# Optimization experiments

Measured on AMD Instinct MI355X. Metric: run time of the kernel, lower is better.

## Reference

```python
import jax, jax.numpy as jnp
import numpy as np
from jax import lax


def conv(x, w, b, stride, pad):
    # x: [B,C,H,W], w: [O,I,kh,kw] (torch layout)
    y = lax.conv_general_dilated(x, w, (stride, stride), ((pad, pad), (pad, pad)),
                                 dimension_numbers=('NCHW', 'OIHW', 'NCHW'))
    return y + b[None, :, None, None]


def convT(x, w, b, stride, pad):
    # torch ConvTranspose2d weight layout [in, out, kh, kw]
    k = w.shape[2]
    wf = jnp.flip(w, (2, 3)).transpose(1, 0, 2, 3)  # -> [out, in, kh, kw]
    p = k - 1 - pad
    y = lax.conv_general_dilated(x, wf, (1, 1), ((p, p), (p, p)),
                                 lhs_dilation=(stride, stride),
                                 dimension_numbers=('NCHW', 'OIHW', 'NCHW'))
    return y + b[None, :, None, None]


def resblock(x, wa, ba, wb, bb):
    h = conv(jax.nn.relu(x), wa, ba, 1, 1)   # 3x3
    h2 = conv(jax.nn.relu(h), wb, bb, 1, 0)  # 1x1
    return x + h2


def vqvae_forward(x, e1_w, e1_b, e2_w, e2_b, e3_w, e3_b,
                  er1a_w, er1a_b, er1b_w, er1b_b, er2a_w, er2a_b, er2b_w, er2b_b,
                  codebook,
                  d1_w, d1_b, dr1a_w, dr1a_b, dr1b_w, dr1b_b,
                  dr2a_w, dr2a_b, dr2b_w, dr2b_b,
                  dt1_w, dt1_b, dt2_w, dt2_b):
    # encoder
    h = jax.nn.relu(conv(x, e1_w, e1_b, 2, 1))
    h = jax.nn.relu(conv(h, e2_w, e2_b, 2, 1))
    h = conv(h, e3_w, e3_b, 1, 1)
    h = resblock(h, er1a_w, er1a_b, er1b_w, er1b_b)
    ze = resblock(h, er2a_w, er2a_b, er2b_w, er2b_b)  # [B,C,H,W]
    # VQ: nearest codebook vector per spatial location (squared L2)
    zef = ze.transpose(0, 2, 3, 1)  # [B,H,W,C]
    # ||z - e||^2 = ||z||^2 - 2 z.e + ||e||^2 (same argmin as explicit broadcast)
    d = (jnp.sum(zef * zef, -1, keepdims=True)
         - 2.0 * jnp.einsum('bhwc,kc->bhwk', zef, codebook)
         + jnp.sum(codebook * codebook, -1))  # [B,H,W,K]
    idx = jnp.argmin(d, -1)                    # [B,H,W]
    zq = codebook[idx].transpose(0, 3, 1, 2)   # [B,C,H,W]
    # straight-through estimator
    dec_in = ze + lax.stop_gradient(zq - ze)
    # decoder
    g = conv(dec_in, d1_w, d1_b, 1, 1)
    g = resblock(g, dr1a_w, dr1a_b, dr1b_w, dr1b_b)
    g = resblock(g, dr2a_w, dr2a_b, dr2b_w, dr2b_b)
    g = jax.nn.relu(convT(g, dt1_w, dt1_b, 2, 1))
    x_hat = convT(g, dt2_w, dt2_b, 2, 1)
    return x_hat, ze, zq


def setup_inputs() -> dict:
    key = jax.random.key(0)
    ks = iter(jax.random.split(key, 64))
    C, K = 128, 512

    def w(shape, scale=0.02):
        return jax.random.normal(next(ks), shape, jnp.float32) * scale

    inp = {}
    inp['x'] = jax.random.normal(next(ks), (16, 3, 256, 256), jnp.float32)
    inp['e1_w'] = w((C, 3, 4, 4)); inp['e1_b'] = w((C,))
    inp['e2_w'] = w((C, C, 4, 4)); inp['e2_b'] = w((C,))
    inp['e3_w'] = w((C, C, 3, 3)); inp['e3_b'] = w((C,))
    inp['er1a_w'] = w((C, C, 3, 3)); inp['er1a_b'] = w((C,))
    inp['er1b_w'] = w((C, C, 1, 1)); inp['er1b_b'] = w((C,))
    inp['er2a_w'] = w((C, C, 3, 3)); inp['er2a_b'] = w((C,))
    inp['er2b_w'] = w((C, C, 1, 1)); inp['er2b_b'] = w((C,))
    inp['codebook'] = jax.random.uniform(next(ks), (K, C), jnp.float32, -1.0 / K, 1.0 / K)
    inp['d1_w'] = w((C, C, 3, 3)); inp['d1_b'] = w((C,))
    inp['dr1a_w'] = w((C, C, 3, 3)); inp['dr1a_b'] = w((C,))
    inp['dr1b_w'] = w((C, C, 1, 1)); inp['dr1b_b'] = w((C,))
    inp['dr2a_w'] = w((C, C, 3, 3)); inp['dr2a_b'] = w((C,))
    inp['dr2b_w'] = w((C, C, 1, 1)); inp['dr2b_b'] = w((C,))
    inp['dt1_w'] = w((C, C, 4, 4)); inp['dt1_b'] = w((C,))   # ConvTranspose [in,out,kh,kw]
    inp['dt2_w'] = w((C, 3, 4, 4)); inp['dt2_b'] = w((3,))
    return inp


def reference(x, e1_w, e1_b, e2_w, e2_b, e3_w, e3_b,
              er1a_w, er1a_b, er1b_w, er1b_b, er2a_w, er2a_b, er2b_w, er2b_b,
              codebook,
              d1_w, d1_b, dr1a_w, dr1a_b, dr1b_w, dr1b_b,
              dr2a_w, dr2a_b, dr2b_w, dr2b_b,
              dt1_w, dt1_b, dt2_w, dt2_b):
    return vqvae_forward(x, e1_w, e1_b, e2_w, e2_b, e3_w, e3_b,
                         er1a_w, er1a_b, er1b_w, er1b_b, er2a_w, er2a_b, er2b_w, er2b_b,
                         codebook,
                         d1_w, d1_b, dr1a_w, dr1a_b, dr1b_w, dr1b_b,
                         dr2a_w, dr2a_b, dr2b_w, dr2b_b,
                         dt1_w, dt1_b, dt2_w, dt2_b)
```

## Files before the change

kernel.cpp:

```cpp
#include <hip/hip_runtime.h>
#include <stdint.h>

typedef unsigned short u16;
typedef __attribute__((ext_vector_type(8))) short short8;
typedef __attribute__((ext_vector_type(4))) float floatx4;

#define RS66  (66*128)
#define IS66  (66*66*128)
#define RS130 (130*128)
#define IS130 (130*130*128)

__device__ __forceinline__ float bf2f(u16 h) {
  union { unsigned u; float f; } v; v.u = ((unsigned)h) << 16; return v.f;
}
__device__ __forceinline__ u16 f2bf(float f) {
  union { float f; unsigned u; } v; v.f = f;
  unsigned r = v.u + 0x7FFFu + ((v.u >> 16) & 1u);
  return (u16)(r >> 16);
}
__device__ __forceinline__ void gl_lds16(const void* g, void* l) {
  __builtin_amdgcn_global_load_lds(
      (const __attribute__((address_space(1))) void*)(uintptr_t)g,
      (__attribute__((address_space(3))) void*)(uintptr_t)l, 16, 0, 0);
}
__device__ __forceinline__ unsigned fkey(float f) {
  unsigned u = __float_as_uint(f);
  return (u & 0x80000000u) ? ~u : (u | 0x80000000u);
}

struct Taps { int n; unsigned dh2; unsigned dw2; };

__global__ __launch_bounds__(256) void conv_mfma(
    const u16* __restrict__ in, int inRS, int inIS, int si,
    const u16* __restrict__ wt, const float* __restrict__ bias, Taps tp,
    u16* __restrict__ out, int outRS, int outIS, int so, int oh0, int ow0,
    const u16* __restrict__ res, u16* __restrict__ out2, int reluMain,
    float* __restrict__ zeOut, u16* __restrict__ zeBFc)
{
  __shared__ u16 lA[4096];
  __shared__ u16 lB[4096];
  const int tid = threadIdx.x;
  const int w = tid >> 6, lane = tid & 63, quad = lane >> 4, l16 = lane & 15;
  const int wm = w >> 1, wn = w & 1;
  const int q = tid & 3, p0 = tid >> 2;
  const int blockM = blockIdx.x << 7;
  const int pg0 = blockM + p0, pg1 = pg0 + 64;
  const int b0 = pg0 >> 12, mo0 = (pg0 >> 6) & 63, no0 = pg0 & 63;
  const int b1 = pg1 >> 12, mo1 = (pg1 >> 6) & 63, no1 = pg1 & 63;
  const u16* gA0 = in + b0*inIS + si*mo0*inRS + si*no0*128 + q*8;
  const u16* gA1 = in + b1*inIS + si*mo1*inRS + si*no1*128 + q*8;
  const u16* gB0 = wt + p0*128 + q*8;
  const u16* gB1 = gB0 + 64*128;
  u16* lsA0 = lA + w*512; u16* lsA1 = lsA0 + 2048;
  u16* lsB0 = lB + w*512; u16* lsB1 = lsB0 + 2048;

  floatx4 zz = {0.f,0.f,0.f,0.f};
  floatx4 acc[4][4];
#pragma unroll
  for (int i=0;i<4;i++)
#pragma unroll
    for (int j=0;j<4;j++) acc[i][j] = zz;

  for (int t = 0; t < tp.n; ++t) {
    const int dh = (int)((tp.dh2 >> (2*t)) & 3u) - 1;
    const int dw = (int)((tp.dw2 >> (2*t)) & 3u) - 1;
    const int aoff = dh*inRS + dw*128;
    const int boff = t << 14;
#pragma unroll
    for (int kc = 0; kc < 4; ++kc) {
      __syncthreads();
      gl_lds16(gA0 + aoff + kc*32, lsA0);
      gl_lds16(gA1 + aoff + kc*32, lsA1);
      gl_lds16(gB0 + boff + kc*32, lsB0);
      gl_lds16(gB1 + boff + kc*32, lsB1);
      __syncthreads();
      short8 af[4], bfr[4];
#pragma unroll
      for (int s=0;s<4;s++) af[s]  = *(const short8*)&lA[(wm*64 + s*16 + l16)*32 + quad*8];
#pragma unroll
      for (int s=0;s<4;s++) bfr[s] = *(const short8*)&lB[(wn*64 + s*16 + l16)*32 + quad*8];
#pragma unroll
      for (int i=0;i<4;i++)
#pragma unroll
        for (int j=0;j<4;j++)
          acc[i][j] = __builtin_amdgcn_mfma_f32_16x16x32_bf16(af[i], bfr[j], acc[i][j], 0, 0, 0);
    }
  }

  float bv[4];
#pragma unroll
  for (int j=0;j<4;j++) bv[j] = bias[wn*64 + j*16 + l16];

#pragma unroll
  for (int i=0;i<4;i++) {
#pragma unroll
    for (int r=0;r<4;r++) {
      const int p = blockM + wm*64 + i*16 + quad*4 + r;
      const int bb = p >> 12, mo = (p >> 6) & 63, no = p & 63;
      const int ob = bb*outIS + (so*mo + oh0)*outRS + (so*no + ow0)*128;
#pragma unroll
      for (int j=0;j<4;j++) {
        const int n = wn*64 + j*16 + l16;
        float v = acc[i][j][r] + bv[j];
        if (res)  v += bf2f(res[ob + n]);
        if (out)  out[ob + n]  = f2bf(reluMain ? fmaxf(v, 0.f) : v);
        if (out2) out2[ob + n] = f2bf(fmaxf(v, 0.f));
        if (zeOut) {
          zeOut[(((size_t)bb) << 19) + ((size_t)n << 12) + (p & 4095)] = v;
          zeBFc[((size_t)p << 7) + n] = f2bf(v);
        }
      }
    }
  }
}

__global__ __launch_bounds__(256) void vq_score(
    const u16* __restrict__ zeBF, const u16* __restrict__ cbBF,
    const float* __restrict__ cbn, unsigned long long* __restrict__ minbuf)
{
  __shared__ u16 lA[4096];
  __shared__ u16 lB[4096];
  const int tid = threadIdx.x;
  const int w = tid >> 6, lane = tid & 63, quad = lane >> 4, l16 = lane & 15;
  const int wm = w >> 1, wn = w & 1;
  const int q = tid & 3, p0 = tid >> 2;
  const int blockM = blockIdx.x << 7;
  const int nb = blockIdx.y;
  const u16* gA0 = zeBF + ((blockM + p0) << 7) + q*8;
  const u16* gA1 = gA0 + (64 << 7);
  const u16* gB0 = cbBF + ((nb*128 + p0) << 7) + q*8;
  const u16* gB1 = gB0 + (64 << 7);
  u16* lsA0 = lA + w*512; u16* lsA1 = lsA0 + 2048;
  u16* lsB0 = lB + w*512; u16* lsB1 = lsB0 + 2048;

  floatx4 zz = {0.f,0.f,0.f,0.f};
  floatx4 acc[4][4];
#pragma unroll
  for (int i=0;i<4;i++)
#pragma unroll
    for (int j=0;j<4;j++) acc[i][j] = zz;

#pragma unroll
  for (int kc = 0; kc < 4; ++kc) {
    __syncthreads();
    gl_lds16(gA0 + kc*32, lsA0);
    gl_lds16(gA1 + kc*32, lsA1);
    gl_lds16(gB0 + kc*32, lsB0);
    gl_lds16(gB1 + kc*32, lsB1);
    __syncthreads();
    short8 af[4], bfr[4];
#pragma unroll
    for (int s=0;s<4;s++) af[s]  = *(const short8*)&lA[(wm*64 + s*16 + l16)*32 + quad*8];
#pragma unroll
    for (int s=0;s<4;s++) bfr[s] = *(const short8*)&lB[(wn*64 + s*16 + l16)*32 + quad*8];
#pragma unroll
    for (int i=0;i<4;i++)
#pragma unroll
      for (int j=0;j<4;j++)
        acc[i][j] = __builtin_amdgcn_mfma_f32_16x16x32_bf16(af[i], bfr[j], acc[i][j], 0, 0, 0);
  }

  float cn[4];
#pragma unroll
  for (int j=0;j<4;j++) cn[j] = cbn[nb*128 + wn*64 + j*16 + l16];

#pragma unroll
  for (int i=0;i<4;i++) {
#pragma unroll
    for (int r=0;r<4;r++) {
      const int p = blockM + wm*64 + i*16 + quad*4 + r;
      unsigned long long best = 0xFFFFFFFFFFFFFFFFull;
#pragma unroll
      for (int j=0;j<4;j++) {
        const int n = nb*128 + wn*64 + j*16 + l16;
        float v = cn[j] - acc[i][j][r];
        unsigned long long pk = ((unsigned long long)fkey(v) << 32) | (unsigned)n;
        if (pk < best) best = pk;
      }
#pragma unroll
      for (int d=1; d<16; d<<=1) {
        unsigned long long o = __shfl_xor(best, d, 64);
        if (o < best) best = o;
      }
      if (l16 == 0) atomicMin(minbuf + p, best);
    }
  }
}

__global__ __launch_bounds__(256) void zq_out_k(
    const unsigned long long* __restrict__ minb, const float* __restrict__ cb,
    float* __restrict__ outZ, u16* __restrict__ zqI)
{
  int id = blockIdx.x*256 + threadIdx.x;
  int c = id & 127, p = id >> 7;
  int n = (int)(unsigned)(minb[p] & 0xFFFFFFFFull);
  float v = cb[(n << 7) + c];
  int b = p >> 12, hw = p & 4095;
  outZ[(((size_t)b) << 19) + ((size_t)c << 12) + hw] = v;
  int h = hw >> 6, w2 = hw & 63;
  zqI[b*IS66 + h*RS66 + w2*128 + c] = f2bf(v);
}

__global__ __launch_bounds__(256) void zero_halos(
    u16* big, u16* s0, u16* s1, u16* s2, u16* s3, unsigned long long* minb)
{
  int id = blockIdx.x*256 + threadIdx.x;
  if (id >= 463872) return;
  if (id >= 398336) { minb[id - 398336] = 0xFFFFFFFFFFFFFFFFull; return; }
  u16* base; int H, W;
  if (id < 132096) { base = big; H = 128; W = 128; }
  else {
    id -= 132096;
    int bi = id / 66560;
    id -= bi*66560;
    base = (bi == 0) ? s0 : (bi == 1) ? s1 : (bi == 2) ? s2 : s3;
    H = 64; W = 64;
  }
  int Wp = W+2, Hp = H+2;
  int cv = id & 15; int rest = id >> 4;
  int npx = 2*Wp + 2*H;
  int img = rest / npx; int pix = rest - img*npx;
  int hh, wwp;
  if (pix < Wp) { hh = 0; wwp = pix; }
  else if (pix < 2*Wp) { hh = Hp-1; wwp = pix - Wp; }
  else { int r2 = pix - 2*Wp; hh = 1 + (r2 >> 1); wwp = (r2 & 1) ? (Wp-1) : 0; }
  uint4 zv = {0u,0u,0u,0u};
  *(uint4*)(base + (((size_t)img*Hp + hh)*Wp + wwp)*128 + cv*8) = zv;
}

struct WEnt { const float* src; u16* dst; int O, I, T, mode; };
struct WTab { int n; WEnt e[16]; int cum[17]; };
__global__ __launch_bounds__(256) void prep_w(WTab wt) {
  int id = blockIdx.x*256 + threadIdx.x;
  if (id >= wt.cum[wt.n]) return;
  int k = 0;
  while (id >= wt.cum[k+1]) k++;
  int l = id - wt.cum[k];
  WEnt E = wt.e[k];
  if (E.mode == 0) {
    int i = l % E.I; int rest = l / E.I; int o = rest % E.O; int t = rest / E.O;
    E.dst[l] = f2bf(E.src[(o*E.I + i)*E.T + t]);
  } else if (E.mode == 1) {
    int i = l & 127, o = (l >> 7) & 127, tt = (l >> 14) & 3, cls = l >> 16;
    int th = tt >> 1, tw = tt & 1, po = cls >> 1, pw = cls & 1;
    int kh = po ? (th ? 2 : 0) : (th ? 3 : 1);
    int kw = pw ? (tw ? 2 : 0) : (tw ? 3 : 1);
    E.dst[l] = f2bf(E.src[((i*128 + o)*4 + kh)*4 + kw]);
  } else if (E.mode == 2) {
    E.dst[l] = f2bf(E.src[l]);
  } else if (E.mode == 3) {
    float s = 0.f; const float* r = E.src + l*128;
    for (int c=0;c<128;c++) s += r[c]*r[c];
    ((float*)E.dst)[l] = 0.5f*s;
  } else if (E.mode == 4) {
    int o = l & 127, tap = l >> 7;
    ((float*)E.dst)[l] = E.src[o*48 + tap];
  } else {
    int c = l & 127, n = l >> 7;
    int o = n >> 4, kk = n & 15;
    E.dst[l] = f2bf(E.src[c*48 + o*16 + kk]);
  }
}

__global__ __launch_bounds__(256) void conv_e1(
    const float* __restrict__ x, const float* __restrict__ wT,
    const float* __restrict__ bias, u16* __restrict__ outI)
{
  __shared__ float inS[12*260];
  __shared__ float wS[48*128];
  __shared__ float bS[128];
  const int tid = threadIdx.x;
  const int b = blockIdx.x >> 7, ho = blockIdx.x & 127;

  for (int l = tid; l < 1536; l += 256)
    ((float4*)wS)[l] = ((const float4*)wT)[l];
  if (tid < 128) bS[tid] = bias[tid];
  for (int l = tid; l < 3120; l += 256) {
    int col = l % 260; int rest = l / 260;
    int kh = rest & 3, c = rest >> 2;
    int hi = 2*ho + kh - 1, wi = col - 1;
    float v = 0.f;
    if ((unsigned)hi < 256u && (unsigned)wi < 256u)
      v = x[((b*3 + c) << 16) + (hi << 8) + wi];
    inS[rest*260 + col] = v;
  }
  __syncthreads();

  const int g = tid & 7;
  const int pxg = tid >> 3;
  floatx4 acc[4][4];
  {
    const floatx4* bp = (const floatx4*)&bS[g*16];
    floatx4 b0 = bp[0], b1 = bp[1], b2 = bp[2], b3 = bp[3];
#pragma unroll
    for (int px=0;px<4;px++) { acc[px][0]=b0; acc[px][1]=b1; acc[px][2]=b2; acc[px][3]=b3; }
  }
#pragma unroll
  for (int c=0;c<3;c++)
#pragma unroll
    for (int kh=0;kh<4;kh++) {
      const float* row = &inS[(c*4+kh)*260];
#pragma unroll
      for (int kw=0;kw<4;kw++) {
        const int tap = c*16 + kh*4 + kw;
        const floatx4* wp = (const floatx4*)&wS[tap*128 + g*16];
        floatx4 w0 = wp[0], w1 = wp[1], w2 = wp[2], w3 = wp[3];
#pragma unroll
        for (int px=0;px<4;px++) {
          float xv = row[((pxg*4 + px) << 1) + kw];
          acc[px][0] += xv*w0; acc[px][1] += xv*w1;
          acc[px][2] += xv*w2; acc[px][3] += xv*w3;
        }
      }
    }

  u16* ob = outI + b*IS130 + ho*RS130;
#pragma unroll
  for (int px=0;px<4;px++) {
    const int wo = pxg*4 + px;
    u16* p = ob + wo*128 + g*16;
#pragma unroll
    for (int k=0;k<4;k++) {
      union { u16 u[4]; uint2 v2; } pk;
#pragma unroll
      for (int j=0;j<4;j++) pk.u[j] = f2bf(fmaxf(acc[px][k][j], 0.f));
      *(uint2*)(p + k*4) = pk.v2;
    }
  }
}

__global__ __launch_bounds__(256) void dt2_gemm(
    const u16* __restrict__ inI, const u16* __restrict__ Wb,
    float* __restrict__ cols)
{
  const int tid = threadIdx.x;
  const int w = tid >> 6, lane = tid & 63, quad = lane >> 4, l16 = lane & 15;
  const int pixBase = blockIdx.x*256 + w*64;

  short8 Bf[3][4];
#pragma unroll
  for (int nt=0; nt<3; nt++)
#pragma unroll
    for (int kc=0; kc<4; kc++)
      Bf[nt][kc] = *(const short8*)(Wb + (nt*16 + l16)*128 + kc*32 + quad*8);

  const u16* ap[4];
#pragma unroll
  for (int ms=0; ms<4; ms++) {
    int p = pixBase + ms*16 + l16;
    int b = p >> 14, rem = p & 16383;
    ap[ms] = inI + b*IS130 + (rem >> 7)*RS130 + (rem & 127)*128;
  }

  floatx4 zz = {0.f,0.f,0.f,0.f};
  floatx4 acc[4][3];
#pragma unroll
  for (int ms=0; ms<4; ms++)
#pragma unroll
    for (int nt=0; nt<3; nt++) acc[ms][nt] = zz;

#pragma unroll
  for (int kc=0; kc<4; kc++) {
#pragma unroll
    for (int ms=0; ms<4; ms++) {
      short8 a = *(const short8*)(ap[ms] + kc*32 + quad*8);
#pragma unroll
      for (int nt=0; nt<3; nt++)
        acc[ms][nt] = __builtin_amdgcn_mfma_f32_16x16x32_bf16(a, Bf[nt][kc], acc[ms][nt], 0, 0, 0);
    }
  }

#pragma unroll
  for (int ms=0; ms<4; ms++)
#pragma unroll
    for (int nt=0; nt<3; nt++)
#pragma unroll
      for (int r=0; r<4; r++) {
        int p = pixBase + ms*16 + quad*4 + r;
        cols[(size_t)p*48 + nt*16 + l16] = acc[ms][nt][r];
      }
}

__global__ __launch_bounds__(256) void dt2_gather(
    const float* __restrict__ cols, const float* __restrict__ bias,
    float* __restrict__ xhat)
{
  int id = blockIdx.x*256 + threadIdx.x;
  int b = id >> 16, rem = id & 65535;
  int ho = rem >> 8, wo = rem & 255;
  const int ph = ho & 1, pw = wo & 1;
  const int hi0 = ph ? ((ho+1)>>1) : (ho>>1);
  const int kh0 = ph ? 0 : 1;
  const int wi0 = pw ? ((wo+1)>>1) : (wo>>1);
  const int kw0 = pw ? 0 : 1;
  float a0 = bias[0], a1 = bias[1], a2 = bias[2];
#pragma unroll
  for (int th=0; th<2; th++) {
    const int hi = hi0 - th;
    if ((unsigned)hi >= 128u) continue;
    const int kh = kh0 + 2*th;
#pragma unroll
    for (int tw=0; tw<2; tw++) {
      const int wi = wi0 - tw;
      if ((unsigned)wi >= 128u) continue;
      const int kw = kw0 + 2*tw;
      const float* r = cols + (size_t)((b << 14) + (hi << 7) + wi)*48 + (kh*4 + kw);
      a0 += r[0]; a1 += r[16]; a2 += r[32];
    }
  }
  const int ob = ((b*3) << 16) + (ho << 8) + wo;
  xhat[ob]          = a0;
  xhat[ob + 65536]  = a1;
  xhat[ob + 131072] = a2;
}

extern "C" void kernel_launch(void* const* d_in, const int* in_sizes, int n_in,
                              void* d_out, int out_size, void* d_ws, size_t ws_size,
                              hipStream_t stream)
{
  const float* x     = (const float*)d_in[0];
  const float* e1w   = (const float*)d_in[1];
  const float* e1b   = (const float*)d_in[2];
  const float* e2w   = (const float*)d_in[3];
  const float* e2b   = (const float*)d_in[4];
  const float* e3w   = (const float*)d_in[5];
  const float* e3b   = (const float*)d_in[6];
  const float* er1aw = (const float*)d_in[7];
  const float* er1ab = (const float*)d_in[8];
  const float* er1bw = (const float*)d_in[9];
  const float* er1bb = (const float*)d_in[10];
  const float* er2aw = (const float*)d_in[11];
  const float* er2ab = (const float*)d_in[12];
  const float* er2bw = (const float*)d_in[13];
  const float* er2bb = (const float*)d_in[14];
  const float* cb    = (const float*)d_in[15];
  const float* d1w   = (const float*)d_in[16];
  const float* d1b   = (const float*)d_in[17];
  const float* dr1aw = (const float*)d_in[18];
  const float* dr1ab = (const float*)d_in[19];
  const float* dr1bw = (const float*)d_in[20];
  const float* dr1bb = (const float*)d_in[21];
  const float* dr2aw = (const float*)d_in[22];
  const float* dr2ab = (const float*)d_in[23];
  const float* dr2bw = (const float*)d_in[24];
  const float* dr2bb = (const float*)d_in[25];
  const float* dt1w  = (const float*)d_in[26];
  const float* dt1b  = (const float*)d_in[27];
  const float* dt2w  = (const float*)d_in[28];
  const float* dt2b  = (const float*)d_in[29];
  float* out = (float*)d_out;

  char* ws = (char*)d_ws;
  size_t off = 0;
  auto alloc = [&](size_t bytes) -> void* {
    void* r = ws + off; off += (bytes + 255) & ~(size_t)255; return r;
  };

  u16* BIG = (u16*)alloc((size_t)IS130*16*2);
  u16* S[4];
  for (int i=0;i<4;i++) S[i] = (u16*)alloc((size_t)IS66*16*2);
  unsigned long long* minb = (unsigned long long*)alloc((size_t)65536*8);
  u16* W_e2 = (u16*)alloc(262144*2);
  u16* W9[6]; for (int i=0;i<6;i++) W9[i] = (u16*)alloc(147456*2);
  u16* W1[4]; for (int i=0;i<4;i++) W1[i] = (u16*)alloc(16384*2);
  u16* Wdt1 = (u16*)alloc(262144*2);
  u16* cbBF = (u16*)alloc(65536*2);
  float* cbn = (float*)alloc(512*4);
  float* wsE1 = (float*)alloc(6144*4);
  u16* Wb48 = (u16*)alloc(6144*2);

  u16* BIGi = BIG + RS130 + 128;
  u16* Si[4];
  for (int i=0;i<4;i++) Si[i] = S[i] + RS66 + 128;
  u16* zeBFc = S[1];
  float* cols = (float*)S[1];

  zero_halos<<<1812, 256, 0, stream>>>(BIG, S[0], S[1], S[2], S[3], minb);

  WTab wtab; int ne = 0; wtab.cum[0] = 0;
  auto addw = [&](const float* s, u16* d, int O, int I, int T, int m, int items) {
    wtab.e[ne] = {s, d, O, I, T, m};
    wtab.cum[ne+1] = wtab.cum[ne] + items; ne++;
  };
  addw(e2w,   W_e2, 128,128,16,0, 262144);
  addw(e3w,   W9[0],128,128, 9,0, 147456);
  addw(er1aw, W9[1],128,128, 9,0, 147456);
  addw(er2aw, W9[2],128,128, 9,0, 147456);
  addw(d1w,   W9[3],128,128, 9,0, 147456);
  addw(dr1aw, W9[4],128,128, 9,0, 147456);
  addw(dr2aw, W9[5],128,128, 9,0, 147456);
  addw(er1bw, W1[0],128,128, 1,0, 16384);
  addw(er2bw, W1[1],128,128, 1,0, 16384);
  addw(dr1bw, W1[2],128,128, 1,0, 16384);
  addw(dr2bw, W1[3],128,128, 1,0, 16384);
  addw(dt1w,  Wdt1, 0,0,0,1, 262144);
  addw(cb,    cbBF, 0,0,0,2, 65536);
  addw(cb,    (u16*)cbn, 0,0,0,3, 512);
  addw(e1w,   (u16*)wsE1, 0,0,0,4, 6144);
  addw(dt2w,  Wb48, 0,0,0,5, 6144);
  wtab.n = ne;
  prep_w<<<(wtab.cum[ne] + 255)/256, 256, 0, stream>>>(wtab);

  conv_e1<<<2048, 256, 0, stream>>>(x, wsE1, e1b, BIGi);

  Taps t16; t16.n = 16; t16.dh2 = 0; t16.dw2 = 0;
  for (int t=0;t<16;t++) { t16.dh2 |= (unsigned)(t>>2) << (2*t); t16.dw2 |= (unsigned)(t&3) << (2*t); }
  Taps t9; t9.n = 9; t9.dh2 = 0; t9.dw2 = 0;
  for (int t=0;t<9;t++) { t9.dh2 |= (unsigned)(t/3) << (2*t); t9.dw2 |= (unsigned)(t%3) << (2*t); }
  Taps t1x; t1x.n = 1; t1x.dh2 = 1; t1x.dw2 = 1;
  Taps tc[4];
  for (int cls=0; cls<4; ++cls) {
    int po = cls >> 1, pw = cls & 1;
    tc[cls].n = 4; tc[cls].dh2 = 0; tc[cls].dw2 = 0;
    for (int tt=0; tt<4; ++tt) {
      int th = tt >> 1, tw = tt & 1;
      int dh = po ? (th ? 0 : 1) : (th ? -1 : 0);
      int dw = pw ? (tw ? 0 : 1) : (tw ? -1 : 0);
      tc[cls].dh2 |= (unsigned)(dh+1) << (2*tt);
      tc[cls].dw2 |= (unsigned)(dw+1) << (2*tt);
    }
  }

  auto conv = [&](const u16* in_, int iRS, int iIS, int si,
                  const u16* w_, const float* b_, Taps tp,
                  u16* o_, int oRS, int oIS, int so, int oh, int ow,
                  const u16* r_, u16* o2, int rl, float* zf, u16* zb) {
    conv_mfma<<<512, 256, 0, stream>>>(in_, iRS, iIS, si, w_, b_, tp,
                                       o_, oRS, oIS, so, oh, ow, r_, o2, rl, zf, zb);
  };

  conv(BIGi, RS130, IS130, 2, W_e2, e2b, t16, Si[0], RS66, IS66, 1,0,0, nullptr, nullptr, 1, nullptr, nullptr);
  conv(Si[0], RS66, IS66, 1, W9[0], e3b, t9, Si[1], RS66, IS66, 1,0,0, nullptr, Si[2], 0, nullptr, nullptr);
  conv(Si[2], RS66, IS66, 1, W9[1], er1ab, t9, Si[0], RS66, IS66, 1,0,0, nullptr, nullptr, 1, nullptr, nullptr);
  conv(Si[0], RS66, IS66, 1, W1[0], er1bb, t1x, Si[3], RS66, IS66, 1,0,0, Si[1], Si[2], 0, nullptr, nullptr);
  conv(Si[2], RS66, IS66, 1, W9[2], er2ab, t9, Si[0], RS66, IS66, 1,0,0, nullptr, nullptr, 1, nullptr, nullptr);
  conv(Si[0], RS66, IS66, 1, W1[1], er2bb, t1x, nullptr, RS66, IS66, 1,0,0, Si[3], nullptr, 0,
       out + 3145728, zeBFc);

  vq_score<<<dim3(512,4), 256, 0, stream>>>(zeBFc, cbBF, cbn, minb);
  zq_out_k<<<32768, 256, 0, stream>>>(minb, cb, out + 11534336, Si[2]);

  conv(Si[2], RS66, IS66, 1, W9[3], d1b, t9, Si[0], RS66, IS66, 1,0,0, nullptr, Si[1], 0, nullptr, nullptr);
  conv(Si[1], RS66, IS66, 1, W9[4], dr1ab, t9, Si[2], RS66, IS66, 1,0,0, nullptr, nullptr, 1, nullptr, nullptr);
  conv(Si[2], RS66, IS66, 1, W1[2], dr1bb, t1x, Si[3], RS66, IS66, 1,0,0, Si[0], Si[1], 0, nullptr, nullptr);
  conv(Si[1], RS66, IS66, 1, W9[5], dr2ab, t9, Si[2], RS66, IS66, 1,0,0, nullptr, nullptr, 1, nullptr, nullptr);
  conv(Si[2], RS66, IS66, 1, W1[3], dr2bb, t1x, Si[0], RS66, IS66, 1,0,0, Si[3], nullptr, 0, nullptr, nullptr);

  for (int cls=0; cls<4; ++cls) {
    int po = cls >> 1, pw = cls & 1;
    conv(Si[0], RS66, IS66, 1, Wdt1 + cls*65536, dt1b, tc[cls],
         BIGi, RS130, IS130, 2, po, pw, nullptr, nullptr, 1, nullptr, nullptr);
  }

  dt2_gemm<<<1024, 256, 0, stream>>>(BIGi, Wb48, cols);
  dt2_gather<<<4096, 256, 0, stream>>>(cols, dt2b, out);
}
```

Measured before the change: 796.0 us.

## Coalesce ze output via LDS-transposed finalize kernel and batch convT launches

The last encoder conv now writes ze channel-last in fp32 to a scratch buffer instead of scattered NCHW stores. A new finalize kernel transposes it through shared memory to produce the NCHW ze and zq outputs plus the bf16 padded zq input, replacing the per-element zq_out kernel. The four transposed-conv parity launches are merged into one launch with a 2D grid, where each blockIdx.y picks its taps and weight slice. This adds an extra fp32 round trip through the BIG buffer, which is reused as scratch before it is overwritten later.

```diff
diff --git a/kernel.cpp b/kernel.cpp
--- a/kernel.cpp
+++ b/kernel.cpp
@@ -35,7 +35,7 @@
     const u16* __restrict__ wt, const float* __restrict__ bias, Taps tp,
     u16* __restrict__ out, int outRS, int outIS, int so, int oh0, int ow0,
     const u16* __restrict__ res, u16* __restrict__ out2, int reluMain,
-    float* __restrict__ zeOut, u16* __restrict__ zeBFc)
+    float* __restrict__ zeFc, u16* __restrict__ zeBFc, int multi)
 {
   __shared__ u16 lA[4096];
   __shared__ u16 lB[4096];
@@ -44,6 +44,16 @@
   const int wm = w >> 1, wn = w & 1;
   const int q = tid & 3, p0 = tid >> 2;
   const int blockM = blockIdx.x << 7;
+
+  unsigned dh2 = tp.dh2, dw2 = tp.dw2;
+  if (multi) {
+    const int cls = blockIdx.y;
+    dh2 = (tp.dh2 >> (8*cls)) & 0xffu;
+    dw2 = (tp.dw2 >> (8*cls)) & 0xffu;
+    wt += cls << 16;
+    oh0 = cls >> 1; ow0 = cls & 1;
+  }
+
   const int pg0 = blockM + p0, pg1 = pg0 + 64;
   const int b0 = pg0 >> 12, mo0 = (pg0 >> 6) & 63, no0 = pg0 & 63;
   const int b1 = pg1 >> 12, mo1 = (pg1 >> 6) & 63, no1 = pg1 & 63;
@@ -62,8 +72,8 @@
     for (int j=0;j<4;j++) acc[i][j] = zz;
 
   for (int t = 0; t < tp.n; ++t) {
-    const int dh = (int)((tp.dh2 >> (2*t)) & 3u) - 1;
-    const int dw = (int)((tp.dw2 >> (2*t)) & 3u) - 1;
+    const int dh = (int)((dh2 >> (2*t)) & 3u) - 1;
+    const int dw = (int)((dw2 >> (2*t)) & 3u) - 1;
     const int aoff = dh*inRS + dw*128;
     const int boff = t << 14;
 #pragma unroll
@@ -105,8 +115,8 @@
         if (res)  v += bf2f(res[ob + n]);
         if (out)  out[ob + n]  = f2bf(reluMain ? fmaxf(v, 0.f) : v);
         if (out2) out2[ob + n] = f2bf(fmaxf(v, 0.f));
-        if (zeOut) {
-          zeOut[(((size_t)bb) << 19) + ((size_t)n << 12) + (p & 4095)] = v;
+        if (zeFc) {
+          zeFc[((size_t)p << 7) + n] = v;
           zeBFc[((size_t)p << 7) + n] = f2bf(v);
         }
       }
@@ -187,18 +197,39 @@
   }
 }
 
-__global__ __launch_bounds__(256) void zq_out_k(
-    const unsigned long long* __restrict__ minb, const float* __restrict__ cb,
-    float* __restrict__ outZ, u16* __restrict__ zqI)
-{
-  int id = blockIdx.x*256 + threadIdx.x;
-  int c = id & 127, p = id >> 7;
-  int n = (int)(unsigned)(minb[p] & 0xFFFFFFFFull);
-  float v = cb[(n << 7) + c];
-  int b = p >> 12, hw = p & 4095;
-  outZ[(((size_t)b) << 19) + ((size_t)c << 12) + hw] = v;
-  int h = hw >> 6, w2 = hw & 63;
-  zqI[b*IS66 + h*RS66 + w2*128 + c] = f2bf(v);
+__global__ __launch_bounds__(256) void finalize(
+    const float* __restrict__ zeFc, const unsigned long long* __restrict__ minb,
+    const float* __restrict__ cb, float* __restrict__ outZe, float* __restrict__ outZq,
+    u16* __restrict__ zqI)
+{
+  __shared__ float T[64*129];
+  __shared__ int ns[64];
+  const int tid = threadIdx.x;
+  const int P0 = blockIdx.x << 6;
+  const int b = P0 >> 12, hw0 = P0 & 4095;
+
+#pragma unroll
+  for (int it=0; it<32; ++it) {
+    int e = it*256 + tid;
+    int px = e >> 7, c = e & 127;
+    T[px*129 + c] = zeFc[((size_t)P0 << 7) + e];
+  }
+  if (tid < 64) ns[tid] = (int)(unsigned)(minb[P0 + tid] & 0xFFFFFFFFull);
+  __syncthreads();
+
+  float* zeB = outZe + (((size_t)b) << 19) + hw0;
+  float* zqB = outZq + (((size_t)b) << 19) + hw0;
+  const int h = hw0 >> 6;
+  u16* zqIB = zqI + b*IS66 + h*RS66;
+#pragma unroll
+  for (int it=0; it<32; ++it) {
+    const int c = it*4 + (tid >> 6);
+    const int px = tid & 63;
+    zeB[(c << 12) + px] = T[px*129 + c];
+    float v = cb[(ns[px] << 7) + c];
+    zqB[(c << 12) + px] = v;
+    zqIB[px*128 + c] = f2bf(v);
+  }
 }
 
 __global__ __launch_bounds__(256) void zero_halos(
@@ -473,6 +504,7 @@
   u16* Si[4];
   for (int i=0;i<4;i++) Si[i] = S[i] + RS66 + 128;
   u16* zeBFc = S[1];
+  float* zeFc = (float*)BIG;
   float* cols = (float*)S[1];
 
   zero_halos<<<1812, 256, 0, stream>>>(BIG, S[0], S[1], S[2], S[3], minb);
@@ -508,16 +540,15 @@
   Taps t9; t9.n = 9; t9.dh2 = 0; t9.dw2 = 0;
   for (int t=0;t<9;t++) { t9.dh2 |= (unsigned)(t/3) << (2*t); t9.dw2 |= (unsigned)(t%3) << (2*t); }
   Taps t1x; t1x.n = 1; t1x.dh2 = 1; t1x.dw2 = 1;
-  Taps tc[4];
+  Taps tcm; tcm.n = 4; tcm.dh2 = 0; tcm.dw2 = 0;
   for (int cls=0; cls<4; ++cls) {
     int po = cls >> 1, pw = cls & 1;
-    tc[cls].n = 4; tc[cls].dh2 = 0; tc[cls].dw2 = 0;
     for (int tt=0; tt<4; ++tt) {
       int th = tt >> 1, tw = tt & 1;
       int dh = po ? (th ? 0 : 1) : (th ? -1 : 0);
       int dw = pw ? (tw ? 0 : 1) : (tw ? -1 : 0);
-      tc[cls].dh2 |= (unsigned)(dh+1) << (2*tt);
-      tc[cls].dw2 |= (unsigned)(dw+1) << (2*tt);
+      tcm.dh2 |= (unsigned)(dh+1) << (8*cls + 2*tt);
+      tcm.dw2 |= (unsigned)(dw+1) << (8*cls + 2*tt);
     }
   }
 
@@ -526,7 +557,7 @@
                   u16* o_, int oRS, int oIS, int so, int oh, int ow,
                   const u16* r_, u16* o2, int rl, float* zf, u16* zb) {
     conv_mfma<<<512, 256, 0, stream>>>(in_, iRS, iIS, si, w_, b_, tp,
-                                       o_, oRS, oIS, so, oh, ow, r_, o2, rl, zf, zb);
+                                       o_, oRS, oIS, so, oh, ow, r_, o2, rl, zf, zb, 0);
   };
 
   conv(BIGi, RS130, IS130, 2, W_e2, e2b, t16, Si[0], RS66, IS66, 1,0,0, nullptr, nullptr, 1, nullptr, nullptr);
@@ -534,11 +565,10 @@
   conv(Si[2], RS66, IS66, 1, W9[1], er1ab, t9, Si[0], RS66, IS66, 1,0,0, nullptr, nullptr, 1, nullptr, nullptr);
   conv(Si[0], RS66, IS66, 1, W1[0], er1bb, t1x, Si[3], RS66, IS66, 1,0,0, Si[1], Si[2], 0, nullptr, nullptr);
   conv(Si[2], RS66, IS66, 1, W9[2], er2ab, t9, Si[0], RS66, IS66, 1,0,0, nullptr, nullptr, 1, nullptr, nullptr);
-  conv(Si[0], RS66, IS66, 1, W1[1], er2bb, t1x, nullptr, RS66, IS66, 1,0,0, Si[3], nullptr, 0,
-       out + 3145728, zeBFc);
+  conv(Si[0], RS66, IS66, 1, W1[1], er2bb, t1x, nullptr, RS66, IS66, 1,0,0, Si[3], nullptr, 0, zeFc, zeBFc);
 
   vq_score<<<dim3(512,4), 256, 0, stream>>>(zeBFc, cbBF, cbn, minb);
-  zq_out_k<<<32768, 256, 0, stream>>>(minb, cb, out + 11534336, Si[2]);
+  finalize<<<1024, 256, 0, stream>>>(zeFc, minb, cb, out + 3145728, out + 11534336, Si[2]);
 
   conv(Si[2], RS66, IS66, 1, W9[3], d1b, t9, Si[0], RS66, IS66, 1,0,0, nullptr, Si[1], 0, nullptr, nullptr);
   conv(Si[1], RS66, IS66, 1, W9[4], dr1ab, t9, Si[2], RS66, IS66, 1,0,0, nullptr, nullptr, 1, nullptr, nullptr);
@@ -546,11 +576,9 @@
   conv(Si[1], RS66, IS66, 1, W9[5], dr2ab, t9, Si[2], RS66, IS66, 1,0,0, nullptr, nullptr, 1, nullptr, nullptr);
   conv(Si[2], RS66, IS66, 1, W1[3], dr2bb, t1x, Si[0], RS66, IS66, 1,0,0, Si[3], nullptr, 0, nullptr, nullptr);
 
-  for (int cls=0; cls<4; ++cls) {
-    int po = cls >> 1, pw = cls & 1;
-    conv(Si[0], RS66, IS66, 1, Wdt1 + cls*65536, dt1b, tc[cls],
-         BIGi, RS130, IS130, 2, po, pw, nullptr, nullptr, 1, nullptr, nullptr);
-  }
+  conv_mfma<<<dim3(512,4), 256, 0, stream>>>(Si[0], RS66, IS66, 1, Wdt1, dt1b, tcm,
+                                             BIGi, RS130, IS130, 2, 0, 0,
+                                             nullptr, nullptr, 1, nullptr, nullptr, 1);
 
   dt2_gemm<<<1024, 256, 0, stream>>>(BIGi, Wb48, cols);
   dt2_gather<<<4096, 256, 0, stream>>>(cols, dt2b, out);
```

New measurement: 747.2 us. 6.1% less time.
